# Performance work log

Measured on AMD Instinct MI355X. Metric: run time of the kernel, lower is better.

The kernel has to match this reference:

```python
import jax, jax.numpy as jnp
import numpy as np

N, E = 50000, 1600000
F_IN, EDGE_DIM, HID, HEADS, NCLS = 64, 16, 128, 4, 40
C = HID // HEADS  # per-head dim = 32


def setup_inputs() -> dict:
    key = jax.random.key(0)
    ks = jax.random.split(key, 20)
    s = 0.1
    inp = {
        'x': jax.random.normal(ks[0], (N, F_IN), jnp.float32),
        'edge_index': jax.random.randint(ks[1], (2, E), 0, N, jnp.int64),
        'edge_attr': jax.random.normal(ks[2], (E, EDGE_DIM), jnp.float32),
        # layer 1 params
        'W1': jax.random.normal(ks[3], (HID, F_IN), jnp.float32) * s,
        'as1': jax.random.normal(ks[4], (HEADS, C), jnp.float32) * s,
        'ad1': jax.random.normal(ks[5], (HEADS, C), jnp.float32) * s,
        'ae1': jax.random.normal(ks[6], (HEADS, C), jnp.float32) * s,
        'We1': jax.random.normal(ks[7], (HID, EDGE_DIM), jnp.float32) * s,
        'b1': jnp.zeros((HID,), jnp.float32),
        # layer 2 params
        'W2': jax.random.normal(ks[8], (HID, HID), jnp.float32) * s,
        'as2': jax.random.normal(ks[9], (HEADS, C), jnp.float32) * s,
        'ad2': jax.random.normal(ks[10], (HEADS, C), jnp.float32) * s,
        'ae2': jax.random.normal(ks[11], (HEADS, C), jnp.float32) * s,
        'We2': jax.random.normal(ks[12], (HID, EDGE_DIM), jnp.float32) * s,
        'b2': jnp.zeros((HID,), jnp.float32),
        # final classifier
        'Wlin': jax.random.normal(ks[13], (NCLS, HID), jnp.float32) * s,
        'blin': jnp.zeros((NCLS,), jnp.float32),
    }
    return inp


def gat_conv(x, src, dst, eattr, W, a_s, a_d, a_e, We, b):
    """PyG GATConv (concat=True, add_self_loops=True, fill_value='mean'), eval mode."""
    n = x.shape[0]
    H, Cd = a_s.shape
    h = (x @ W.T).reshape(n, H, Cd)  # [N,H,C]
    # self-loop edge_attr = per-destination mean of incoming edge_attr
    cnt = jax.ops.segment_sum(jnp.ones((dst.shape[0],), eattr.dtype), dst, num_segments=n)
    mean_ea = jax.ops.segment_sum(eattr, dst, num_segments=n) / jnp.maximum(cnt, 1.0)[:, None]
    loops = jnp.arange(n, dtype=src.dtype)
    s_idx = jnp.concatenate([src, loops])
    d_idx = jnp.concatenate([dst, loops])
    ea = jnp.concatenate([eattr, mean_ea], axis=0)  # [E+N, edge_dim]
    e = (ea @ We.T).reshape(-1, H, Cd)
    # edge-wise attention logits
    alpha = (h * a_s).sum(-1)[s_idx] + (h * a_d).sum(-1)[d_idx] + (e * a_e).sum(-1)  # [E+N,H]
    alpha = jax.nn.leaky_relu(alpha, 0.2)
    # segment softmax over destination neighborhoods (every node has a self-loop)
    amax = jax.ops.segment_max(alpha, d_idx, num_segments=n)
    ex = jnp.exp(alpha - amax[d_idx])
    den = jax.ops.segment_sum(ex, d_idx, num_segments=n)
    coef = ex / (den[d_idx] + 1e-16)
    out = jax.ops.segment_sum(h[s_idx] * coef[:, :, None], d_idx, num_segments=n)
    return out.reshape(n, H * Cd) + b


def reference(x, edge_index, edge_attr, W1, as1, ad1, ae1, We1, b1,
              W2, as2, ad2, ae2, We2, b2, Wlin, blin):
    src, dst = edge_index[0], edge_index[1]
    h = jax.nn.relu(gat_conv(x, src, dst, edge_attr, W1, as1, ad1, ae1, We1, b1))
    h = jax.nn.relu(gat_conv(h, src, dst, edge_attr, W2, as2, ad2, ae2, We2, b2))
    logits = h @ Wlin.T + blin
    return jax.nn.log_softmax(logits, axis=1)
```

## Files before the change

### kernel.cpp

```cpp
#include <hip/hip_runtime.h>
#include <hip/hip_bf16.h>
#include <math.h>


#define CHUNK 8192
#define CAPC 12288

typedef __attribute__((ext_vector_type(8))) short short8;
typedef __attribute__((ext_vector_type(4))) float floatx4;

__device__ __forceinline__ unsigned short f2bf(float f) {
  unsigned u = __float_as_uint(f);
  unsigned r = u + 0x7FFFu + ((u >> 16) & 1u);
  return (unsigned short)(r >> 16);
}
__device__ __forceinline__ float bf2f(unsigned short b) {
  return __uint_as_float(((unsigned)b) << 16);
}

__global__ __launch_bounds__(512) void hist_kernel(const int* __restrict__ dst,
                                                   int* __restrict__ bucketCnt,
                                                   int E, int NB) {
  __shared__ int hist[512];
  const int tid = threadIdx.x;
  hist[tid] = 0;
  __syncthreads();
  const int e0 = blockIdx.x * CHUNK, e1 = min(e0 + CHUNK, E);
  for (int e = e0 + tid; e < e1; e += 512) atomicAdd(&hist[dst[e] >> 7], 1);
  __syncthreads();
  if (tid < NB && hist[tid]) atomicAdd(&bucketCnt[tid], hist[tid]);
}

__global__ __launch_bounds__(512) void scanB_kernel(const int* __restrict__ bucketCnt,
                                                    int* __restrict__ bucketOffs,
                                                    int* __restrict__ bucketPos,
                                                    int* __restrict__ offs,
                                                    int NB, int N, int E) {
  __shared__ int sc[512];
  const int tid = threadIdx.x;
  const int v = (tid < NB) ? bucketCnt[tid] : 0;
  sc[tid] = v;
  __syncthreads();
  for (int off = 1; off < 512; off <<= 1) {
    int t = (tid >= off) ? sc[tid - off] : 0;
    __syncthreads();
    sc[tid] += t;
    __syncthreads();
  }
  const int excl = sc[tid] - v;
  if (tid < NB) { bucketOffs[tid] = excl; bucketPos[tid] = excl; }
  if (tid == 0) { bucketOffs[NB] = E; offs[N] = E; }
}

__global__ __launch_bounds__(512) void partB_kernel(const int* __restrict__ src,
                                                    const int* __restrict__ dst,
                                                    int* __restrict__ bucketPos,
                                                    int2* __restrict__ binned,
                                                    int E, int NB) {
  __shared__ int hist[512], sc[512], lbase[513], gbase[512], lcnt[512];
  __shared__ int2 stage[CHUNK];
  const int tid = threadIdx.x;
  const int e0 = blockIdx.x * CHUNK;
  const int e1 = min(e0 + CHUNK, E);
  hist[tid] = 0; lcnt[tid] = 0;
  __syncthreads();
  for (int e = e0 + tid; e < e1; e += 512) atomicAdd(&hist[dst[e] >> 7], 1);
  __syncthreads();
  sc[tid] = hist[tid];
  __syncthreads();
  for (int off = 1; off < 512; off <<= 1) {
    int t = (tid >= off) ? sc[tid - off] : 0;
    __syncthreads();
    sc[tid] += t;
    __syncthreads();
  }
  lbase[tid + 1] = sc[tid];
  if (tid == 0) lbase[0] = 0;
  if (tid < NB && hist[tid] > 0) gbase[tid] = atomicAdd(&bucketPos[tid], hist[tid]);
  __syncthreads();
  for (int e = e0 + tid; e < e1; e += 512) {
    const int d = dst[e];
    const int b = d >> 7;
    const int lr = atomicAdd(&lcnt[b], 1);
    int2 v;
    v.x = src[e];
    v.y = (int)(((unsigned)(d & 127) << 25) | (unsigned)e);
    stage[lbase[b] + lr] = v;
  }
  __syncthreads();
  const int total = e1 - e0;
  for (int t = tid; t < total; t += 512) {
    int lo = 0, hi = 511;
    while (lo < hi) {
      int mid = (lo + hi + 1) >> 1;
      if (lbase[mid] <= t) lo = mid; else hi = mid - 1;
    }
    binned[gbase[lo] + (t - lbase[lo])] = stage[t];
  }
}

__global__ __launch_bounds__(256) void passC_kernel(const int2* __restrict__ binned,
                                                    const int* __restrict__ bucketOffs,
                                                    int* __restrict__ srcS,
                                                    int* __restrict__ elist,
                                                    int* __restrict__ offs, int N) {
  __shared__ int cnt[128], dbase[129], dpos[128];
  __shared__ int2 stage[CAPC];
  const int tid = threadIdx.x;
  const int b = blockIdx.x;
  const int bo = bucketOffs[b], be = bucketOffs[b + 1];
  const int m = be - bo;
  if (tid < 128) { cnt[tid] = 0; dpos[tid] = 0; }
  __syncthreads();
  for (int t = tid; t < m; t += 256) {
    int2 v = binned[bo + t];
    if (t < CAPC) stage[t] = v;
    atomicAdd(&cnt[((unsigned)v.y) >> 25], 1);
  }
  __syncthreads();
  for (int off = 1; off < 128; off <<= 1) {
    int t = (tid < 128 && tid >= (unsigned)off) ? cnt[tid - off] : 0;
    __syncthreads();
    if (tid < 128) cnt[tid] += t;
    __syncthreads();
  }
  if (tid == 0) dbase[0] = 0;
  if (tid < 128) dbase[tid + 1] = cnt[tid];
  __syncthreads();
  const int dcnt = min(128, N - (b << 7));
  if (tid < dcnt) offs[(b << 7) + tid] = bo + dbase[tid];
  for (int t = tid; t < m; t += 256) {
    int2 v = (t < CAPC) ? stage[t] : binned[bo + t];
    const unsigned py = (unsigned)v.y;
    const int dl = py >> 25;
    const int p = dbase[dl] + atomicAdd(&dpos[dl], 1);
    srcS[bo + p] = v.x;
    elist[bo + p] = (int)(py & 0x1FFFFFFu);
  }
}

__global__ __launch_bounds__(128) void wa_kernel(const float* __restrict__ ae1,
                                                 const float* __restrict__ We1,
                                                 const float* __restrict__ ae2,
                                                 const float* __restrict__ We2,
                                                 float* __restrict__ Wa) {
  int t = threadIdx.x;
  const float* ae = (t < 64) ? ae1 : ae2;
  const float* We = (t < 64) ? We1 : We2;
  int h = (t >> 4) & 3;
  int d = t & 15;
  float s = 0.f;
  for (int c = 0; c < 32; ++c) s += ae[h * 32 + c] * We[(h * 32 + c) * 16 + d];
  Wa[t] = s;
}

__global__ __launch_bounds__(256) void cvt3_kernel(const float* __restrict__ a,
                                                   unsigned short* __restrict__ ao, int na,
                                                   const float* __restrict__ b,
                                                   unsigned short* __restrict__ bo, int nb,
                                                   const float* __restrict__ c,
                                                   unsigned short* __restrict__ co, int nc) {
  int i = blockIdx.x * 256 + threadIdx.x;
  if (i < na) ao[i] = f2bf(a[i]);
  else if (i < na + nb) bo[i - na] = f2bf(b[i - na]);
  else if (i < na + nb + nc) co[i - na - nb] = f2bf(c[i - na - nb]);
}

__global__ __launch_bounds__(256) void alphae12_kernel(const int* __restrict__ elist,
                                                       const float* __restrict__ ea,
                                                       const float* __restrict__ Wa,
                                                       unsigned short* __restrict__ ae1s,
                                                       unsigned short* __restrict__ ae2s,
                                                       int E) {
  __shared__ float wa[128];
  if (threadIdx.x < 128) wa[threadIdx.x] = Wa[threadIdx.x];
  __syncthreads();
  int j = blockIdx.x * 256 + threadIdx.x;
  if (j >= E) return;
  const int e = elist[j];
  const float4* p = (const float4*)(ea + (size_t)e * 16);
  float4 q0 = p[0], q1 = p[1], q2 = p[2], q3 = p[3];
  float v[16] = {q0.x, q0.y, q0.z, q0.w, q1.x, q1.y, q1.z, q1.w,
                 q2.x, q2.y, q2.z, q2.w, q3.x, q3.y, q3.z, q3.w};
  unsigned short rr[8];
#pragma unroll
  for (int h = 0; h < 8; ++h) {
    float s = 0.f;
#pragma unroll
    for (int d = 0; d < 16; ++d) s += v[d] * wa[h * 16 + d];
    rr[h] = f2bf(s);
  }
  ushort4 lo; lo.x = rr[0]; lo.y = rr[1]; lo.z = rr[2]; lo.w = rr[3];
  ushort4 hi; hi.x = rr[4]; hi.y = rr[5]; hi.z = rr[6]; hi.w = rr[7];
  *(ushort4*)(ae1s + (size_t)j * 4) = lo;
  *(ushort4*)(ae2s + (size_t)j * 4) = hi;
}

__global__ __launch_bounds__(256) void gemm_mfma_kernel(const unsigned short* __restrict__ X,
                                                        const unsigned short* __restrict__ Wb,
                                                        unsigned short* __restrict__ H,
                                                        int n, int K) {
  const int w = threadIdx.x >> 6;
  const int lane = threadIdx.x & 63;
  const int m0 = blockIdx.x * 64;
  const int quad = lane >> 4;
  const int l15 = lane & 15;
  floatx4 acc[4][2];
#pragma unroll
  for (int mt = 0; mt < 4; ++mt)
#pragma unroll
    for (int nt = 0; nt < 2; ++nt) acc[mt][nt] = (floatx4)(0.f);

  int rowm[4];
#pragma unroll
  for (int mt = 0; mt < 4; ++mt) {
    int r = m0 + mt * 16 + l15;
    rowm[mt] = (r < n) ? r : (n - 1);
  }
  const int ncol0 = (w << 5) + l15;

  for (int kc = 0; kc < K; kc += 32) {
    const int koff = kc + (quad << 3);
    short8 a[4], b[2];
#pragma unroll
    for (int mt = 0; mt < 4; ++mt)
      a[mt] = *(const short8*)(X + (size_t)rowm[mt] * K + koff);
#pragma unroll
    for (int nt = 0; nt < 2; ++nt)
      b[nt] = *(const short8*)(Wb + (size_t)(ncol0 + nt * 16) * K + koff);
#pragma unroll
    for (int mt = 0; mt < 4; ++mt)
#pragma unroll
      for (int nt = 0; nt < 2; ++nt)
        acc[mt][nt] = __builtin_amdgcn_mfma_f32_16x16x32_bf16(a[mt], b[nt], acc[mt][nt], 0, 0, 0);
  }
#pragma unroll
  for (int mt = 0; mt < 4; ++mt) {
    const int rbase = m0 + mt * 16 + (quad << 2);
#pragma unroll
    for (int nt = 0; nt < 2; ++nt) {
      const int col = ncol0 + nt * 16;
#pragma unroll
      for (int r = 0; r < 4; ++r) {
        const int row = rbase + r;
        if (row < n) H[(size_t)row * 128 + col] = f2bf(acc[mt][nt][r]);
      }
    }
  }
}

__global__ __launch_bounds__(256) void score_kernel(const unsigned short* __restrict__ h,
                                                    const float* __restrict__ a_s,
                                                    const float* __restrict__ a_d,
                                                    float* __restrict__ ssc,
                                                    float* __restrict__ dsc, int n) {
  int gid = blockIdx.x * 256 + threadIdx.x;
  int node = gid >> 6;
  int lane = threadIdx.x & 63;
  if (node >= n) return;
  int ch = lane * 2;
  ushort2 hq = *(const ushort2*)(h + (size_t)node * 128 + ch);
  float h0 = bf2f(hq.x), h1 = bf2f(hq.y);
  float ps = h0 * a_s[ch] + h1 * a_s[ch + 1];
  float pd = h0 * a_d[ch] + h1 * a_d[ch + 1];
#pragma unroll
  for (int off = 8; off; off >>= 1) {
    ps += __shfl_xor(ps, off, 16);
    pd += __shfl_xor(pd, off, 16);
  }
  if ((lane & 15) == 0) {
    int head = lane >> 4;
    ssc[node * 4 + head] = ps;
    dsc[node * 4 + head] = pd;
  }
}

__device__ __forceinline__ float leaky02(float a) { return a > 0.f ? a : 0.2f * a; }
__device__ __forceinline__ float sel4(float4 v, int h) {
  return (h == 0) ? v.x : (h == 1) ? v.y : (h == 2) ? v.z : v.w;
}

__global__ __launch_bounds__(256) void agg_kernel(const unsigned short* __restrict__ hin,
                                                  const float* __restrict__ ssc,
                                                  const float* __restrict__ dsc,
                                                  const unsigned short* __restrict__ aeS,
                                                  const int* __restrict__ offs,
                                                  const int* __restrict__ srcS,
                                                  const float* __restrict__ bias,
                                                  unsigned short* __restrict__ hout, int n) {
  __shared__ int sbuf[4][64];
  __shared__ float pbuf[4][256];
  const int tid = threadIdx.x;
  const int wv = tid >> 6;
  const int lane = tid & 63;
  const int node = blockIdx.x * 4 + wv;
  if (node >= n) return;
  const int l32 = lane & 31;
  const int half = lane >> 5;
  const int ch4 = l32 * 4;
  const int headB = l32 >> 3;
  const float4 dv = *(const float4*)(dsc + (size_t)node * 4);
  float4 l4 = make_float4(0.f, 0.f, 0.f, 0.f);
  float4 sa = make_float4(0.f, 0.f, 0.f, 0.f);
  float acc[4] = {0.f, 0.f, 0.f, 0.f};
  const int j0 = offs[node], j1 = offs[node + 1];

  for (int jc = j0; jc < j1; jc += 64) {
    const int len = min(64, j1 - jc);
    float4 p4 = make_float4(0.f, 0.f, 0.f, 0.f);
    int sv = 0;
    if (lane < len) {
      const int j = jc + lane;
      sv = srcS[j];
      const ushort4 aq = *(const ushort4*)(aeS + (size_t)j * 4);
      const float4 ae4 = make_float4(bf2f(aq.x), bf2f(aq.y), bf2f(aq.z), bf2f(aq.w));
      const float4 ss4 = *(const float4*)(ssc + (size_t)sv * 4);
      sa.x += ae4.x; sa.y += ae4.y; sa.z += ae4.z; sa.w += ae4.w;
      p4.x = __expf(leaky02(ss4.x + dv.x + ae4.x));
      p4.y = __expf(leaky02(ss4.y + dv.y + ae4.y));
      p4.z = __expf(leaky02(ss4.z + dv.z + ae4.z));
      p4.w = __expf(leaky02(ss4.w + dv.w + ae4.w));
    }
    sbuf[wv][lane] = sv;
    *(float4*)(&pbuf[wv][lane * 4]) = p4;
    l4.x += p4.x; l4.y += p4.y; l4.z += p4.z; l4.w += p4.w;
    int k = 0;
    for (; k + 8 <= len; k += 8) {
      int kk0 = k + half, kk1 = k + 2 + half, kk2 = k + 4 + half, kk3 = k + 6 + half;
      int s0 = sbuf[wv][kk0], s1 = sbuf[wv][kk1], s2 = sbuf[wv][kk2], s3 = sbuf[wv][kk3];
      float p0 = pbuf[wv][kk0 * 4 + headB], p1 = pbuf[wv][kk1 * 4 + headB];
      float p2 = pbuf[wv][kk2 * 4 + headB], p3 = pbuf[wv][kk3 * 4 + headB];
      uint2 d0 = *(const uint2*)(hin + (size_t)s0 * 128 + ch4);
      uint2 d1 = *(const uint2*)(hin + (size_t)s1 * 128 + ch4);
      uint2 d2 = *(const uint2*)(hin + (size_t)s2 * 128 + ch4);
      uint2 d3 = *(const uint2*)(hin + (size_t)s3 * 128 + ch4);
      acc[0] += p0 * __uint_as_float(d0.x << 16);
      acc[1] += p0 * __uint_as_float(d0.x & 0xFFFF0000u);
      acc[2] += p0 * __uint_as_float(d0.y << 16);
      acc[3] += p0 * __uint_as_float(d0.y & 0xFFFF0000u);
      acc[0] += p1 * __uint_as_float(d1.x << 16);
      acc[1] += p1 * __uint_as_float(d1.x & 0xFFFF0000u);
      acc[2] += p1 * __uint_as_float(d1.y << 16);
      acc[3] += p1 * __uint_as_float(d1.y & 0xFFFF0000u);
      acc[0] += p2 * __uint_as_float(d2.x << 16);
      acc[1] += p2 * __uint_as_float(d2.x & 0xFFFF0000u);
      acc[2] += p2 * __uint_as_float(d2.y << 16);
      acc[3] += p2 * __uint_as_float(d2.y & 0xFFFF0000u);
      acc[0] += p3 * __uint_as_float(d3.x << 16);
      acc[1] += p3 * __uint_as_float(d3.x & 0xFFFF0000u);
      acc[2] += p3 * __uint_as_float(d3.y << 16);
      acc[3] += p3 * __uint_as_float(d3.y & 0xFFFF0000u);
    }
    for (; k < len; k += 2) {
      int kk = k + half;
      if (kk < len) {
        int s = sbuf[wv][kk];
        float p = pbuf[wv][kk * 4 + headB];
        uint2 d = *(const uint2*)(hin + (size_t)s * 128 + ch4);
        acc[0] += p * __uint_as_float(d.x << 16);
        acc[1] += p * __uint_as_float(d.x & 0xFFFF0000u);
        acc[2] += p * __uint_as_float(d.y << 16);
        acc[3] += p * __uint_as_float(d.y & 0xFFFF0000u);
      }
    }
  }

#pragma unroll
  for (int off = 32; off; off >>= 1) {
    sa.x += __shfl_xor(sa.x, off);
    sa.y += __shfl_xor(sa.y, off);
    sa.z += __shfl_xor(sa.z, off);
    sa.w += __shfl_xor(sa.w, off);
    l4.x += __shfl_xor(l4.x, off);
    l4.y += __shfl_xor(l4.y, off);
    l4.z += __shfl_xor(l4.z, off);
    l4.w += __shfl_xor(l4.w, off);
  }
#pragma unroll
  for (int i = 0; i < 4; ++i) acc[i] += __shfl_xor(acc[i], 32);

  const int deg = j1 - j0;
  const float invd = 1.f / fmaxf((float)deg, 1.f);
  const float ssn = ssc[(size_t)node * 4 + headB];
  const float aloop = leaky02(ssn + sel4(dv, headB) + sel4(sa, headB) * invd);
  const float pl = __expf(aloop);
  const float lF = sel4(l4, headB) + pl;
  const uint2 hd = *(const uint2*)(hin + (size_t)node * 128 + ch4);
  const float hv0 = __uint_as_float(hd.x << 16);
  const float hv1 = __uint_as_float(hd.x & 0xFFFF0000u);
  const float hv2 = __uint_as_float(hd.y << 16);
  const float hv3 = __uint_as_float(hd.y & 0xFFFF0000u);
  const float inv = 1.f / (lF + 1e-16f);
  const float4 bi = *(const float4*)(bias + ch4);
  const float o0 = fmaxf((acc[0] + pl * hv0) * inv + bi.x, 0.f);
  const float o1 = fmaxf((acc[1] + pl * hv1) * inv + bi.y, 0.f);
  const float o2 = fmaxf((acc[2] + pl * hv2) * inv + bi.z, 0.f);
  const float o3 = fmaxf((acc[3] + pl * hv3) * inv + bi.w, 0.f);
  if (half == 0) {
    ushort4 o;
    o.x = f2bf(o0); o.y = f2bf(o1); o.z = f2bf(o2); o.w = f2bf(o3);
    *(ushort4*)(hout + (size_t)node * 128 + ch4) = o;
  }
}

__global__ __launch_bounds__(256) void classifier_kernel(const unsigned short* __restrict__ h,
                                                         const float* __restrict__ Wlin,
                                                         const float* __restrict__ blin,
                                                         float* __restrict__ out, int n) {
  __shared__ float wt[128 * 40];
  __shared__ float hs[4][128];
  for (int idx = threadIdx.x; idx < 40 * 128; idx += 256) {
    int c = idx >> 7, k = idx & 127;
    wt[k * 40 + c] = Wlin[idx];
  }
  int w = threadIdx.x >> 6, lane = threadIdx.x & 63;
  int node = blockIdx.x * 4 + w;
  if (node < n) {
    hs[w][lane] = bf2f(h[(size_t)node * 128 + lane]);
    hs[w][lane + 64] = bf2f(h[(size_t)node * 128 + lane + 64]);
  }
  __syncthreads();
  if (node >= n) return;
  float logit = -INFINITY;
  if (lane < 40) {
    float acc = blin[lane];
#pragma unroll 4
    for (int k = 0; k < 128; ++k) acc += hs[w][k] * wt[k * 40 + lane];
    logit = acc;
  }
  float mx = logit;
#pragma unroll
  for (int off = 32; off; off >>= 1) mx = fmaxf(mx, __shfl_xor(mx, off));
  float ex = (lane < 40) ? __expf(logit - mx) : 0.f;
  float sm = ex;
#pragma unroll
  for (int off = 32; off; off >>= 1) sm += __shfl_xor(sm, off);
  if (lane < 40) out[(size_t)node * 40 + lane] = logit - mx - __logf(sm);
}

extern "C" void kernel_launch(void* const* d_in, const int* in_sizes, int n_in,
                              void* d_out, int out_size, void* d_ws, size_t ws_size,
                              hipStream_t stream) {
  const float* x    = (const float*)d_in[0];
  const int*   eidx = (const int*)d_in[1];
  const float* ea   = (const float*)d_in[2];
  const float* W1   = (const float*)d_in[3];
  const float* as1  = (const float*)d_in[4];
  const float* ad1  = (const float*)d_in[5];
  const float* ae1w = (const float*)d_in[6];
  const float* We1  = (const float*)d_in[7];
  const float* b1   = (const float*)d_in[8];
  const float* W2   = (const float*)d_in[9];
  const float* as2  = (const float*)d_in[10];
  const float* ad2  = (const float*)d_in[11];
  const float* ae2w = (const float*)d_in[12];
  const float* We2  = (const float*)d_in[13];
  const float* b2   = (const float*)d_in[14];
  const float* Wlin = (const float*)d_in[15];
  const float* blin = (const float*)d_in[16];
  float* out = (float*)d_out;

  const int N = in_sizes[0] / 64;
  const int E = in_sizes[1] / 2;
  const int* src = eidx;
  const int* dst = eidx + E;
  const int NB = (N + 127) >> 7;

  char* wsb = (char*)d_ws;
  size_t off = 0;
  auto alloc = [&](size_t bytes) -> void* {
    void* p = wsb + off;
    off = (off + bytes + 255) & ~(size_t)255;
    return p;
  };
  int* bucketCnt  = (int*)alloc(512 * 4);
  int* bucketOffs = (int*)alloc(513 * 4);
  int* bucketPos  = (int*)alloc(512 * 4);
  int* offs       = (int*)alloc((size_t)(N + 1) * 4);
  void* bhA       = alloc((size_t)E * 8 > (size_t)N * 256 ? (size_t)E * 8 : (size_t)N * 256);
  int2* binned    = (int2*)bhA;
  unsigned short* hA = (unsigned short*)bhA;
  int* srcS       = (int*)alloc((size_t)E * 4);
  int* elist      = (int*)alloc((size_t)E * 4);
  float* Wa       = (float*)alloc(128 * 4);
  unsigned short* xb  = (unsigned short*)alloc((size_t)N * 64 * 2);
  unsigned short* Wb1 = (unsigned short*)alloc(128 * 64 * 2);
  unsigned short* Wb2 = (unsigned short*)alloc(128 * 128 * 2);
  float* ssc      = (float*)alloc((size_t)N * 4 * 4);
  float* dsc      = (float*)alloc((size_t)N * 4 * 4);
  unsigned short* ae1s = (unsigned short*)alloc((size_t)E * 4 * 2);
  unsigned short* ae2s = (unsigned short*)alloc((size_t)E * 4 * 2);
  unsigned short* hB   = (unsigned short*)alloc((size_t)N * 128 * 2);

  const int ge = (E + 255) / 256;
  const int gg = (N + 63) / 64;
  const int gn = (N + 3) / 4;
  const int gp = (E + CHUNK - 1) / CHUNK;
  const int ncvt = N * 64 + 128 * 64 + 128 * 128;

  hipMemsetAsync(bucketCnt, 0, 512 * 4, stream);
  hist_kernel<<<gp, 512, 0, stream>>>(dst, bucketCnt, E, NB);
  scanB_kernel<<<1, 512, 0, stream>>>(bucketCnt, bucketOffs, bucketPos, offs, NB, N, E);
  partB_kernel<<<gp, 512, 0, stream>>>(src, dst, bucketPos, binned, E, NB);
  passC_kernel<<<NB, 256, 0, stream>>>(binned, bucketOffs, srcS, elist, offs, N);

  wa_kernel<<<1, 128, 0, stream>>>(ae1w, We1, ae2w, We2, Wa);
  cvt3_kernel<<<(ncvt + 255) / 256, 256, 0, stream>>>(x, xb, N * 64, W1, Wb1, 128 * 64,
                                                      W2, Wb2, 128 * 128);
  alphae12_kernel<<<ge, 256, 0, stream>>>(elist, ea, Wa, ae1s, ae2s, E);

  gemm_mfma_kernel<<<gg, 256, 0, stream>>>(xb, Wb1, hA, N, 64);
  score_kernel<<<gn, 256, 0, stream>>>(hA, as1, ad1, ssc, dsc, N);
  agg_kernel<<<gn, 256, 0, stream>>>(hA, ssc, dsc, ae1s, offs, srcS, b1, hB, N);

  gemm_mfma_kernel<<<gg, 256, 0, stream>>>(hB, Wb2, hA, N, 128);
  score_kernel<<<gn, 256, 0, stream>>>(hA, as2, ad2, ssc, dsc, N);
  agg_kernel<<<gn, 256, 0, stream>>>(hA, ssc, dsc, ae2s, offs, srcS, b2, hB, N);

  classifier_kernel<<<gn, 256, 0, stream>>>(hB, Wlin, blin, out, N);
}
```

Before: 529.6 us.

## Compute classifier logits with bf16 MFMA using hi/lo split weights

Replaces the scalar LDS-based classifier, which used one wave per node and a full Wlin transpose into shared memory per block, with an MFMA kernel that handles 16 rows per wave. The weights are split into bf16 high and low parts so the product keeps near-fp32 accuracy, and a small new kernel builds these padded 48x128 tiles. Log-softmax is done with 16-lane shuffles over the MFMA output layout. The cost is one extra launch and twice the MFMA work for the precision split; the per-block weight staging and scalar FMA loop go away.

```diff
diff --git a/kernel.cpp b/kernel.cpp
--- a/kernel.cpp
+++ b/kernel.cpp
@@ -164,6 +164,17 @@
   if (i < na) ao[i] = f2bf(a[i]);
   else if (i < na + nb) bo[i - na] = f2bf(b[i - na]);
   else if (i < na + nb + nc) co[i - na - nb] = f2bf(c[i - na - nb]);
+}
+
+__global__ __launch_bounds__(256) void cvtw_kernel(const float* __restrict__ Wlin,
+                                                   unsigned short* __restrict__ whi,
+                                                   unsigned short* __restrict__ wlo) {
+  int i = blockIdx.x * 256 + threadIdx.x;
+  if (i >= 48 * 128) return;
+  float v = (i < 40 * 128) ? Wlin[i] : 0.f;
+  unsigned short h = f2bf(v);
+  whi[i] = h;
+  wlo[i] = f2bf(v - bf2f(h));
 }
 
 __global__ __launch_bounds__(256) void alphae12_kernel(const int* __restrict__ elist,
@@ -404,38 +415,58 @@
 }
 
 __global__ __launch_bounds__(256) void classifier_kernel(const unsigned short* __restrict__ h,
-                                                         const float* __restrict__ Wlin,
+                                                         const unsigned short* __restrict__ Whi,
+                                                         const unsigned short* __restrict__ Wlo,
                                                          const float* __restrict__ blin,
                                                          float* __restrict__ out, int n) {
-  __shared__ float wt[128 * 40];
-  __shared__ float hs[4][128];
-  for (int idx = threadIdx.x; idx < 40 * 128; idx += 256) {
-    int c = idx >> 7, k = idx & 127;
-    wt[k * 40 + c] = Wlin[idx];
-  }
-  int w = threadIdx.x >> 6, lane = threadIdx.x & 63;
-  int node = blockIdx.x * 4 + w;
-  if (node < n) {
-    hs[w][lane] = bf2f(h[(size_t)node * 128 + lane]);
-    hs[w][lane + 64] = bf2f(h[(size_t)node * 128 + lane + 64]);
-  }
-  __syncthreads();
-  if (node >= n) return;
-  float logit = -INFINITY;
-  if (lane < 40) {
-    float acc = blin[lane];
-#pragma unroll 4
-    for (int k = 0; k < 128; ++k) acc += hs[w][k] * wt[k * 40 + lane];
-    logit = acc;
-  }
-  float mx = logit;
-#pragma unroll
-  for (int off = 32; off; off >>= 1) mx = fmaxf(mx, __shfl_xor(mx, off));
-  float ex = (lane < 40) ? __expf(logit - mx) : 0.f;
-  float sm = ex;
-#pragma unroll
-  for (int off = 32; off; off >>= 1) sm += __shfl_xor(sm, off);
-  if (lane < 40) out[(size_t)node * 40 + lane] = logit - mx - __logf(sm);
+  const int w = threadIdx.x >> 6;
+  const int lane = threadIdx.x & 63;
+  const int quad = lane >> 4;
+  const int l15 = lane & 15;
+  const int row0 = blockIdx.x * 64 + w * 16;
+  if (row0 >= n) return;
+  int rowm = row0 + l15;
+  if (rowm >= n) rowm = n - 1;
+  floatx4 acc[3];
+#pragma unroll
+  for (int nt = 0; nt < 3; ++nt) acc[nt] = (floatx4)(0.f);
+  const size_t hbase = (size_t)rowm * 128;
+#pragma unroll
+  for (int kc = 0; kc < 128; kc += 32) {
+    const int koff = kc + (quad << 3);
+    short8 a = *(const short8*)(h + hbase + koff);
+#pragma unroll
+    for (int nt = 0; nt < 3; ++nt) {
+      short8 bh = *(const short8*)(Whi + (size_t)(nt * 16 + l15) * 128 + koff);
+      short8 bl = *(const short8*)(Wlo + (size_t)(nt * 16 + l15) * 128 + koff);
+      acc[nt] = __builtin_amdgcn_mfma_f32_16x16x32_bf16(a, bh, acc[nt], 0, 0, 0);
+      acc[nt] = __builtin_amdgcn_mfma_f32_16x16x32_bf16(a, bl, acc[nt], 0, 0, 0);
+    }
+  }
+  const float bl0 = blin[l15];
+  const float bl1 = blin[16 + l15];
+  const float bl2 = (l15 < 8) ? blin[32 + l15] : 0.f;
+#pragma unroll
+  for (int r = 0; r < 4; ++r) {
+    const int rrow = row0 + (quad << 2) + r;
+    const float v0 = acc[0][r] + bl0;
+    const float v1 = acc[1][r] + bl1;
+    const float v2 = (l15 < 8) ? (acc[2][r] + bl2) : -INFINITY;
+    float m = fmaxf(v0, fmaxf(v1, v2));
+#pragma unroll
+    for (int off = 8; off; off >>= 1) m = fmaxf(m, __shfl_xor(m, off, 16));
+    const float e2 = (l15 < 8) ? __expf(v2 - m) : 0.f;
+    float s = __expf(v0 - m) + __expf(v1 - m) + e2;
+#pragma unroll
+    for (int off = 8; off; off >>= 1) s += __shfl_xor(s, off, 16);
+    const float ls = m + __logf(s);
+    if (rrow < n) {
+      float* po = out + (size_t)rrow * 40;
+      po[l15] = v0 - ls;
+      po[16 + l15] = v1 - ls;
+      if (l15 < 8) po[32 + l15] = v2 - ls;
+    }
+  }
 }
 
 extern "C" void kernel_launch(void* const* d_in, const int* in_sizes, int n_in,
@@ -486,6 +517,8 @@
   unsigned short* xb  = (unsigned short*)alloc((size_t)N * 64 * 2);
   unsigned short* Wb1 = (unsigned short*)alloc(128 * 64 * 2);
   unsigned short* Wb2 = (unsigned short*)alloc(128 * 128 * 2);
+  unsigned short* Wlh = (unsigned short*)alloc(48 * 128 * 2);
+  unsigned short* Wll = (unsigned short*)alloc(48 * 128 * 2);
   float* ssc      = (float*)alloc((size_t)N * 4 * 4);
   float* dsc      = (float*)alloc((size_t)N * 4 * 4);
   unsigned short* ae1s = (unsigned short*)alloc((size_t)E * 4 * 2);
@@ -507,6 +540,7 @@
   wa_kernel<<<1, 128, 0, stream>>>(ae1w, We1, ae2w, We2, Wa);
   cvt3_kernel<<<(ncvt + 255) / 256, 256, 0, stream>>>(x, xb, N * 64, W1, Wb1, 128 * 64,
                                                       W2, Wb2, 128 * 128);
+  cvtw_kernel<<<24, 256, 0, stream>>>(Wlin, Wlh, Wll);
   alphae12_kernel<<<ge, 256, 0, stream>>>(elist, ea, Wa, ae1s, ae2s, E);
 
   gemm_mfma_kernel<<<gg, 256, 0, stream>>>(xb, Wb1, hA, N, 64);
@@ -517,5 +551,5 @@
   score_kernel<<<gn, 256, 0, stream>>>(hA, as2, ad2, ssc, dsc, N);
   agg_kernel<<<gn, 256, 0, stream>>>(hA, ssc, dsc, ae2s, offs, srcS, b2, hB, N);
 
-  classifier_kernel<<<gn, 256, 0, stream>>>(hB, Wlin, blin, out, N);
-}
+  classifier_kernel<<<gg, 256, 0, stream>>>(hB, Wlh, Wll, blin, out, N);
+}
```

Result: faster. 483.8 us (-8.7%).
